# Kernel tuning notes

Hardware: AMD Instinct MI355X
Metric: run time of the kernel (lower is better)

The kernel has to match this reference:

```python
import jax, jax.numpy as jnp
import numpy as np
import math

N_LAYERS = 8
D = 1024
H = 16
DK = D // H
T = 1024
V = 32000
B = 2
DFF = 4 * D
EPS = 1e-5


def layernorm(x, scale, bias):
    mu = jnp.mean(x, axis=-1, keepdims=True)
    var = jnp.mean(jnp.square(x - mu), axis=-1, keepdims=True)
    return (x - mu) * jax.lax.rsqrt(var + EPS) * scale + bias


def setup_inputs() -> dict:
    key = jax.random.key(0)
    ks = jax.random.split(key, 32)
    s = 0.02
    rn = lambda k, shape: jax.random.normal(k, shape, dtype=jnp.float32) * s
    x = jax.random.randint(ks[0], (B, T), 0, V)
    return {
        "x": x,
        "inp_emb": rn(ks[1], (V, D)),
        "pos_emb": rn(ks[2], (T, D)),
        # per-layer weights stacked on leading layer axis; per-head wq/wk/wv are
        # concatenated along the output dim (mathematically identical to the
        # per-head nn.Linear list in the torch code)
        "wq": rn(ks[3], (N_LAYERS, D, D)), "bq": jnp.zeros((N_LAYERS, D), jnp.float32),
        "wk": rn(ks[4], (N_LAYERS, D, D)), "bk": jnp.zeros((N_LAYERS, D), jnp.float32),
        "wv": rn(ks[5], (N_LAYERS, D, D)), "bv": jnp.zeros((N_LAYERS, D), jnp.float32),
        "wo": rn(ks[6], (N_LAYERS, D, D)), "bo": jnp.zeros((N_LAYERS, D), jnp.float32),
        "w1": rn(ks[7], (N_LAYERS, D, DFF)), "b1": jnp.zeros((N_LAYERS, DFF), jnp.float32),
        "w2": rn(ks[8], (N_LAYERS, DFF, D)), "b2": jnp.zeros((N_LAYERS, D), jnp.float32),
        "ln1_s": jnp.ones((N_LAYERS, D), jnp.float32), "ln1_b": jnp.zeros((N_LAYERS, D), jnp.float32),
        "ln2_s": jnp.ones((N_LAYERS, D), jnp.float32), "ln2_b": jnp.zeros((N_LAYERS, D), jnp.float32),
        "lno_s": jnp.ones((D,), jnp.float32), "lno_b": jnp.zeros((D,), jnp.float32),
        "w_out": rn(ks[9], (D, V)),
    }


def reference(x, inp_emb, pos_emb, wq, bq, wk, bk, wv, bv, wo, bo,
              w1, b1, w2, b2, ln1_s, ln1_b, ln2_s, ln2_b, lno_s, lno_b, w_out):
    h = inp_emb[x] + pos_emb[jnp.arange(T)]            # [B,T,D]
    causal = jnp.tril(jnp.ones((T, T), dtype=bool))    # [T,T]
    scale = 1.0 / math.sqrt(DK)
    for i in range(N_LAYERS):
        # --- multi-head causal attention ---
        xn = layernorm(h, ln1_s[i], ln1_b[i])
        q = (xn @ wq[i] + bq[i]).reshape(B, T, H, DK)
        k = (xn @ wk[i] + bk[i]).reshape(B, T, H, DK)
        v = (xn @ wv[i] + bv[i]).reshape(B, T, H, DK)
        scores = jnp.einsum('bqhd,bkhd->bhqk', q, k) * scale
        scores = jnp.where(causal, scores, -jnp.inf)
        att = jax.nn.softmax(scores, axis=-1)           # [B,H,T,T]
        y = jnp.einsum('bhqk,bkhd->bqhd', att, v).reshape(B, T, D)
        h = h + y @ wo[i] + bo[i]
        # --- feed-forward ---
        xn = layernorm(h, ln2_s[i], ln2_b[i])
        h = h + jax.nn.gelu(xn @ w1[i] + b1[i], approximate=False) @ w2[i] + b2[i]
    h = layernorm(h, lno_s, lno_b)
    return h @ w_out                                    # logits [B,T,V]
```

## Files before the change

kernel.cpp:

```cpp
#include <hip/hip_runtime.h>
#include <cmath>

#define D_MODEL 1024
#define N_HEADS 16
#define DKH     64
#define SEQ_T   1024
#define BATCH   2
#define VOCAB   32000
#define DFF_    4096
#define NLAYERS 8

typedef __bf16 bf16x8 __attribute__((ext_vector_type(8)));
typedef __bf16 bf16x4v __attribute__((ext_vector_type(4)));
typedef float  f32x4  __attribute__((ext_vector_type(4)));

__device__ __forceinline__ float gelu_f(float x) {
    return 0.5f * x * (1.0f + erff(x * 0.70710678118654752f));
}

__device__ __forceinline__ void gload_lds16(const void* g, void* l) {
    __builtin_amdgcn_global_load_lds(
        (const __attribute__((address_space(1))) void*)g,
        (__attribute__((address_space(3))) void*)l, 16, 0, 0);
}

__global__ __launch_bounds__(256) void embed_kernel(
    const int* __restrict__ x, const float* __restrict__ inp_emb,
    const float* __restrict__ pos_emb, float* __restrict__ h)
{
    const int idx = blockIdx.x * 256 + threadIdx.x;
    const int bt  = idx >> 10;
    const int d   = idx & 1023;
    const int t   = bt & (SEQ_T - 1);
    const int tok = x[bt];
    h[idx] = inp_emb[(size_t)tok * D_MODEL + d] + pos_emb[(size_t)t * D_MODEL + d];
}

__global__ __launch_bounds__(256) void layernorm_kernel(
    const float* __restrict__ x, const float* __restrict__ sc,
    const float* __restrict__ bi, __bf16* __restrict__ o)
{
    const int row = blockIdx.x;
    const int tid = threadIdx.x;
    const int c   = tid * 4;
    const float4 v = *(const float4*)(x + (size_t)row * D_MODEL + c);
    float sum = v.x + v.y + v.z + v.w;
    float sq  = v.x * v.x + v.y * v.y + v.z * v.z + v.w * v.w;
    #pragma unroll
    for (int off = 32; off > 0; off >>= 1) {
        sum += __shfl_xor(sum, off);
        sq  += __shfl_xor(sq, off);
    }
    __shared__ float ssum[4], ssq[4];
    const int wave = tid >> 6, lane = tid & 63;
    if (lane == 0) { ssum[wave] = sum; ssq[wave] = sq; }
    __syncthreads();
    sum = ssum[0] + ssum[1] + ssum[2] + ssum[3];
    sq  = ssq[0]  + ssq[1]  + ssq[2]  + ssq[3];
    const float mu  = sum * (1.0f / D_MODEL);
    const float var = sq * (1.0f / D_MODEL) - mu * mu;
    const float rs  = rsqrtf(var + 1e-5f);
    const float4 s4 = *(const float4*)(sc + c);
    const float4 b4 = *(const float4*)(bi + c);
    bf16x4v ov;
    ov[0] = (__bf16)((v.x - mu) * rs * s4.x + b4.x);
    ov[1] = (__bf16)((v.y - mu) * rs * s4.y + b4.y);
    ov[2] = (__bf16)((v.z - mu) * rs * s4.z + b4.z);
    ov[3] = (__bf16)((v.w - mu) * rs * s4.w + b4.w);
    *(bf16x4v*)(o + (size_t)row * D_MODEL + c) = ov;
}

__global__ __launch_bounds__(256) void prep_layer_kernel(
    const float* __restrict__ wq, const float* __restrict__ wk,
    const float* __restrict__ wv, const float* __restrict__ wo,
    const float* __restrict__ w1, const float* __restrict__ w2,
    const float* __restrict__ bq, const float* __restrict__ bk,
    const float* __restrict__ bv,
    __bf16* __restrict__ wqkvT, __bf16* __restrict__ woT,
    __bf16* __restrict__ w1T, __bf16* __restrict__ w2T,
    float* __restrict__ bqkv)
{
    __shared__ __bf16 tile[32][36];
    const int b   = blockIdx.x;
    const int tid = threadIdx.x;

    if (b >= 12288) {
        const int j = (b - 12288) * 256 + tid;
        bqkv[j] = (j < 1024) ? bq[j] : (j < 2048 ? bk[j - 1024] : bv[j - 2048]);
        return;
    }

    const float* in;
    __bf16* out;
    int K, N, kb0, nb0;
    if (b < 4096) {
        const int w = b >> 10, t = b & 1023;
        K = 1024; N = 1024; kb0 = (t >> 5) * 32; nb0 = (t & 31) * 32;
        in  = (w == 0) ? wq : (w == 1) ? wk : (w == 2) ? wv : wo;
        out = (w == 3) ? woT : wqkvT + (size_t)w * 1024 * 1024;
    } else if (b < 8192) {
        const int t = b - 4096;
        K = 1024; N = 4096; kb0 = (t >> 7) * 32; nb0 = (t & 127) * 32;
        in = w1; out = w1T;
    } else {
        const int t = b - 8192;
        K = 4096; N = 1024; kb0 = (t >> 5) * 32; nb0 = (t & 31) * 32;
        in = w2; out = w2T;
    }

    {
        const int rr = tid >> 3, c4 = (tid & 7) * 4;
        const float4 v = *(const float4*)(in + (size_t)(kb0 + rr) * N + nb0 + c4);
        tile[rr][c4 + 0] = (__bf16)v.x;
        tile[rr][c4 + 1] = (__bf16)v.y;
        tile[rr][c4 + 2] = (__bf16)v.z;
        tile[rr][c4 + 3] = (__bf16)v.w;
    }
    __syncthreads();
    {
        const int cc = tid >> 3, r4 = (tid & 7) * 4;
        bf16x4v ov;
        ov[0] = tile[r4 + 0][cc];
        ov[1] = tile[r4 + 1][cc];
        ov[2] = tile[r4 + 2][cc];
        ov[3] = tile[r4 + 3][cc];
        *(bf16x4v*)(out + (size_t)(nb0 + cc) * K + kb0 + r4) = ov;
    }
}

__global__ __launch_bounds__(256) void wout_tr_kernel(
    const float* __restrict__ in, __bf16* __restrict__ out)
{
    __shared__ __bf16 tile[32][36];
    const int tid = threadIdx.x;
    const int nb0 = (blockIdx.x >> 5) * 32;
    const int kb0 = (blockIdx.x & 31) * 32;
    {
        const int rr = tid >> 3, c4 = (tid & 7) * 4;
        const float4 v = *(const float4*)(in + (size_t)(kb0 + rr) * VOCAB + nb0 + c4);
        tile[rr][c4 + 0] = (__bf16)v.x;
        tile[rr][c4 + 1] = (__bf16)v.y;
        tile[rr][c4 + 2] = (__bf16)v.z;
        tile[rr][c4 + 3] = (__bf16)v.w;
    }
    __syncthreads();
    {
        const int cc = tid >> 3, r4 = (tid & 7) * 4;
        bf16x4v ov;
        ov[0] = tile[r4 + 0][cc];
        ov[1] = tile[r4 + 1][cc];
        ov[2] = tile[r4 + 2][cc];
        ov[3] = tile[r4 + 3][cc];
        *(bf16x4v*)(out + (size_t)(nb0 + cc) * D_MODEL + kb0 + r4) = ov;
    }
}

template <int BN_T, int EPI, typename OutT, bool NT = false>
__global__ __launch_bounds__(256) void gemm_bt(
    const __bf16* __restrict__ A, const __bf16* __restrict__ Bt,
    const float* __restrict__ bias, const float* __restrict__ res,
    OutT* __restrict__ C, int M, int N, int K)
{
    constexpr int NF  = BN_T / 32;
    constexpr int NCB = BN_T / 8;
    __shared__ __bf16 As[128 * 64];
    __shared__ __bf16 Bs[BN_T * 64];

    const int tid  = threadIdx.x;
    const int wave = tid >> 6;
    const int lane = tid & 63;
    const int r    = lane & 15;
    const int kb   = lane >> 4;
    const int wm   = wave >> 1;
    const int wn   = wave & 1;

    const int ntm = gridDim.x;
    const int nwg = ntm * gridDim.y;
    int bid = blockIdx.y * ntm + blockIdx.x;
    if ((nwg & 7) == 0) bid = (bid & 7) * (nwg >> 3) + (bid >> 3);
    const int bm = (bid % ntm) * 128;
    const int bn = (bid / ntm) * BN_T;

    const int srow = lane >> 3;
    const int sg   = lane & 7;

    f32x4 acc[4][NF] = {};

    for (int k0 = 0; k0 < K; k0 += 64) {
        #pragma unroll
        for (int i = 0; i < 4; ++i) {
            const int c    = i * 4 + wave;
            const int row  = c * 8 + srow;
            const int scol = (sg ^ (row & 7)) * 8;
            gload_lds16(A + (size_t)(bm + row) * K + k0 + scol, &As[c * 512]);
        }
        #pragma unroll
        for (int i = 0; i < NCB / 4; ++i) {
            const int c    = i * 4 + wave;
            const int row  = c * 8 + srow;
            const int scol = (sg ^ (row & 7)) * 8;
            gload_lds16(Bt + (size_t)(bn + row) * K + k0 + scol, &Bs[c * 512]);
        }
        __syncthreads();

        #pragma unroll
        for (int s = 0; s < 2; ++s) {
            bf16x8 af[4];
            #pragma unroll
            for (int m = 0; m < 4; ++m) {
                const int row = wm * 64 + m * 16 + r;
                const int g   = (s * 4 + kb) ^ (row & 7);
                af[m] = *(const bf16x8*)&As[row * 64 + g * 8];
            }
            #pragma unroll
            for (int n = 0; n < NF; ++n) {
                const int row = wn * (NF * 16) + n * 16 + r;
                const int g   = (s * 4 + kb) ^ (row & 7);
                const bf16x8 bfr = *(const bf16x8*)&Bs[row * 64 + g * 8];
                #pragma unroll
                for (int m = 0; m < 4; ++m)
                    acc[m][n] = __builtin_amdgcn_mfma_f32_16x16x32_bf16(af[m], bfr, acc[m][n], 0, 0, 0);
            }
        }
        __syncthreads();
    }

    #pragma unroll
    for (int m = 0; m < 4; ++m) {
        const int row = bm + wm * 64 + m * 16 + kb * 4;
        #pragma unroll
        for (int n = 0; n < NF; ++n) {
            const int col = bn + wn * (NF * 16) + n * 16 + r;
            const float bv = bias ? bias[col] : 0.0f;
            #pragma unroll
            for (int rg = 0; rg < 4; ++rg) {
                float v = acc[m][n][rg] + bv;
                if constexpr (EPI == 1) v += res[(size_t)(row + rg) * N + col];
                if constexpr (EPI == 2) v = gelu_f(v);
                if constexpr (NT) {
                    __builtin_nontemporal_store((OutT)v, &C[(size_t)(row + rg) * N + col]);
                } else {
                    C[(size_t)(row + rg) * N + col] = (OutT)v;
                }
            }
        }
    }
}

struct AttnState {
    float m[4];
    float l[4];
    f32x4 yacc[4];
};

template <bool MASK>
__device__ __forceinline__ void attn_tile_step(
    AttnState& st, const bf16x8 (&qf)[2], int q0, int kt,
    int wave, int r, int kb,
    const __bf16 (*K_lds)[72], const __bf16 (*V_lds)[72],
    __bf16 (*P_row)[72])
{
    f32x4 sacc[4] = {};
    #pragma unroll
    for (int kc = 0; kc < 2; ++kc) {
        #pragma unroll
        for (int g = 0; g < 4; ++g) {
            const bf16x8 kf = *(const bf16x8*)&K_lds[g * 16 + r][kc * 32 + kb * 8];
            sacc[g] = __builtin_amdgcn_mfma_f32_16x16x32_bf16(qf[kc], kf, sacc[g], 0, 0, 0);
        }
    }

    float s[4][4], p[4][4];
    #pragma unroll
    for (int g = 0; g < 4; ++g) {
        #pragma unroll
        for (int rg = 0; rg < 4; ++rg) {
            if constexpr (MASK) {
                const int key = kt * 64 + g * 16 + r;
                const int qq  = q0 + wave * 16 + kb * 4 + rg;
                s[g][rg] = (key <= qq) ? sacc[g][rg] * 0.125f : -INFINITY;
            } else {
                s[g][rg] = sacc[g][rg] * 0.125f;
            }
        }
    }

    float mt[4];
    #pragma unroll
    for (int rg = 0; rg < 4; ++rg)
        mt[rg] = fmaxf(fmaxf(s[0][rg], s[1][rg]), fmaxf(s[2][rg], s[3][rg]));
    #pragma unroll
    for (int off = 1; off < 16; off <<= 1) {
        #pragma unroll
        for (int rg = 0; rg < 4; ++rg) mt[rg] = fmaxf(mt[rg], __shfl_xor(mt[rg], off));
    }

    bool grow = false;
    #pragma unroll
    for (int rg = 0; rg < 4; ++rg) grow |= (mt[rg] > st.m[rg] + 8.0f);
    if (__any(grow)) {
        #pragma unroll
        for (int rg = 0; rg < 4; ++rg) {
            const float mn   = fmaxf(st.m[rg], mt[rg]);
            const float corr = __expf(st.m[rg] - mn);
            st.l[rg] *= corr;
            st.m[rg]  = mn;
            #pragma unroll
            for (int n = 0; n < 4; ++n) st.yacc[n][rg] *= corr;
        }
    }

    float psum[4];
    #pragma unroll
    for (int rg = 0; rg < 4; ++rg) {
        psum[rg] = 0.0f;
        #pragma unroll
        for (int g = 0; g < 4; ++g) {
            p[g][rg] = __expf(s[g][rg] - st.m[rg]);
            psum[rg] += p[g][rg];
        }
    }
    #pragma unroll
    for (int off = 1; off < 16; off <<= 1) {
        #pragma unroll
        for (int rg = 0; rg < 4; ++rg) psum[rg] += __shfl_xor(psum[rg], off);
    }
    #pragma unroll
    for (int rg = 0; rg < 4; ++rg) st.l[rg] += psum[rg];

    #pragma unroll
    for (int g = 0; g < 4; ++g) {
        #pragma unroll
        for (int rg = 0; rg < 4; ++rg)
            P_row[kb * 4 + rg][g * 16 + r] = (__bf16)p[g][rg];
    }
    const bf16x8 pa0 = *(const bf16x8*)&P_row[r][kb * 8];
    const bf16x8 pa1 = *(const bf16x8*)&P_row[r][32 + kb * 8];

    #pragma unroll
    for (int n = 0; n < 4; ++n) {
        const int vrow = n * 16 + r;
        const int swz  = (vrow >> 3) & 7;
        const bf16x8 vf0 = *(const bf16x8*)&V_lds[vrow][(kb ^ swz) * 8];
        st.yacc[n] = __builtin_amdgcn_mfma_f32_16x16x32_bf16(pa0, vf0, st.yacc[n], 0, 0, 0);
    }
    #pragma unroll
    for (int n = 0; n < 4; ++n) {
        const int vrow = n * 16 + r;
        const int swz  = (vrow >> 3) & 7;
        const bf16x8 vf1 = *(const bf16x8*)&V_lds[vrow][((kb + 4) ^ swz) * 8];
        st.yacc[n] = __builtin_amdgcn_mfma_f32_16x16x32_bf16(pa1, vf1, st.yacc[n], 0, 0, 0);
    }
}

__global__ __launch_bounds__(256) void attn_mfma_kernel(
    const __bf16* __restrict__ qkv, __bf16* __restrict__ y)
{
    constexpr int QS = 3 * D_MODEL;
    __shared__ __align__(16) __bf16 K_lds[64][72];
    __shared__ __align__(16) __bf16 V_lds[64][72];
    __shared__ __align__(16) __bf16 P_lds[4][16][72];

    const int tid  = threadIdx.x;
    const int wave = tid >> 6;
    const int lane = tid & 63;
    const int r    = lane & 15;
    const int kb   = lane >> 4;

    const int ip  = blockIdx.x;
    const int q0A = ip * 64;
    const int q0B = (15 - ip) * 64;
    const int b   = blockIdx.y >> 4;
    const int h   = blockIdx.y & 15;

    const __bf16* qp = qkv + (size_t)b * SEQ_T * QS + h * DKH;
    const __bf16* kp = qp + D_MODEL;
    const __bf16* vp = qp + 2 * D_MODEL;
    __bf16* yp = y + (size_t)b * SEQ_T * D_MODEL + h * DKH;

    bf16x8 qfA[2], qfB[2];
    {
        const int qrA = q0A + wave * 16 + r;
        const int qrB = q0B + wave * 16 + r;
        #pragma unroll
        for (int kc = 0; kc < 2; ++kc) {
            qfA[kc] = *(const bf16x8*)(qp + (size_t)qrA * QS + kc * 32 + kb * 8);
            qfB[kc] = *(const bf16x8*)(qp + (size_t)qrB * QS + kc * 32 + kb * 8);
        }
    }

    AttnState stA, stB;
    #pragma unroll
    for (int rg = 0; rg < 4; ++rg) {
        stA.m[rg] = -INFINITY; stA.l[rg] = 0.0f;
        stB.m[rg] = -INFINITY; stB.l[rg] = 0.0f;
    }
    #pragma unroll
    for (int n = 0; n < 4; ++n) { stA.yacc[n] = {}; stB.yacc[n] = {}; }

    const int skey = tid >> 2;
    const int sg16 = (tid & 3) * 16;

    const int ntiles = 16 - ip;
    for (int kt = 0; kt < ntiles; ++kt) {
        {
            const size_t go = (size_t)(kt * 64 + skey) * QS;
            *(bf16x8*)&K_lds[skey][sg16]     = *(const bf16x8*)(kp + go + sg16);
            *(bf16x8*)&K_lds[skey][sg16 + 8] = *(const bf16x8*)(kp + go + sg16 + 8);
            const bf16x8 v0 = *(const bf16x8*)(vp + go + sg16);
            const bf16x8 v1 = *(const bf16x8*)(vp + go + sg16 + 8);
            const int swz0 = ((sg16 >> 3) & 7) * 8;
            const int swz1 = (((sg16 + 8) >> 3) & 7) * 8;
            #pragma unroll
            for (int j = 0; j < 8; ++j)
                V_lds[sg16 + j][skey ^ swz0] = v0[j];
            #pragma unroll
            for (int j = 0; j < 8; ++j)
                V_lds[sg16 + 8 + j][skey ^ swz1] = v1[j];
        }
        __syncthreads();

        if (kt == ntiles - 1)
            attn_tile_step<true >(stB, qfB, q0B, kt, wave, r, kb, K_lds, V_lds, P_lds[wave]);
        else
            attn_tile_step<false>(stB, qfB, q0B, kt, wave, r, kb, K_lds, V_lds, P_lds[wave]);
        if (kt <= ip) {
            if (kt == ip)
                attn_tile_step<true >(stA, qfA, q0A, kt, wave, r, kb, K_lds, V_lds, P_lds[wave]);
            else
                attn_tile_step<false>(stA, qfA, q0A, kt, wave, r, kb, K_lds, V_lds, P_lds[wave]);
        }
        __syncthreads();
    }

    float invA[4], invB[4];
    #pragma unroll
    for (int rg = 0; rg < 4; ++rg) {
        invA[rg] = 1.0f / stA.l[rg];
        invB[rg] = 1.0f / stB.l[rg];
    }
    #pragma unroll
    for (int n = 0; n < 4; ++n) {
        #pragma unroll
        for (int rg = 0; rg < 4; ++rg) {
            const int rowA = q0A + wave * 16 + kb * 4 + rg;
            const int rowB = q0B + wave * 16 + kb * 4 + rg;
            yp[(size_t)rowA * D_MODEL + n * 16 + r] = (__bf16)(stA.yacc[n][rg] * invA[rg]);
            yp[(size_t)rowB * D_MODEL + n * 16 + r] = (__bf16)(stB.yacc[n][rg] * invB[rg]);
        }
    }
}

extern "C" void kernel_launch(void* const* d_in, const int* in_sizes, int n_in,
                              void* d_out, int out_size, void* d_ws, size_t ws_size,
                              hipStream_t stream)
{
    const int*   x       = (const int*)  d_in[0];
    const float* inp_emb = (const float*)d_in[1];
    const float* pos_emb = (const float*)d_in[2];
    const float* wq = (const float*)d_in[3];
    const float* bq = (const float*)d_in[4];
    const float* wk = (const float*)d_in[5];
    const float* bk = (const float*)d_in[6];
    const float* wv = (const float*)d_in[7];
    const float* bv = (const float*)d_in[8];
    const float* wo = (const float*)d_in[9];
    const float* bo = (const float*)d_in[10];
    const float* w1 = (const float*)d_in[11];
    const float* b1 = (const float*)d_in[12];
    const float* w2 = (const float*)d_in[13];
    const float* b2 = (const float*)d_in[14];
    const float* ln1_s = (const float*)d_in[15];
    const float* ln1_b = (const float*)d_in[16];
    const float* ln2_s = (const float*)d_in[17];
    const float* ln2_b = (const float*)d_in[18];
    const float* lno_s = (const float*)d_in[19];
    const float* lno_b = (const float*)d_in[20];
    const float* w_out = (const float*)d_in[21];

    const int M = BATCH * SEQ_T;
    const size_t MB = 1u << 20;

    char* w = (char*)d_ws;
    float*  h     = (float*) (w + 0);
    __bf16* xn    = (__bf16*)(w + 8  * MB);
    __bf16* yb    = (__bf16*)(w + 12 * MB);
    __bf16* sh    = (__bf16*)(w + 16 * MB);
    __bf16* wqkvT = (__bf16*)(w + 32 * MB);
    __bf16* woT   = (__bf16*)(w + 38 * MB);
    __bf16* w1T   = (__bf16*)(w + 40 * MB);
    __bf16* w2T   = (__bf16*)(w + 48 * MB);
    float*  bqkv  = (float*) (w + 56 * MB);
    __bf16* woutT = (__bf16*)(w + 57 * MB);

    embed_kernel<<<dim3(M * D_MODEL / 256), 256, 0, stream>>>(x, inp_emb, pos_emb, h);

    for (int i = 0; i < NLAYERS; ++i) {
        const size_t wOff  = (size_t)i * D_MODEL * D_MODEL;
        const size_t w1Off = (size_t)i * D_MODEL * DFF_;

        prep_layer_kernel<<<dim3(12300), 256, 0, stream>>>(
            wq + wOff, wk + wOff, wv + wOff, wo + wOff, w1 + w1Off, w2 + w1Off,
            bq + i * D_MODEL, bk + i * D_MODEL, bv + i * D_MODEL,
            wqkvT, woT, w1T, w2T, bqkv);

        layernorm_kernel<<<dim3(M), 256, 0, stream>>>(h, ln1_s + i * D_MODEL, ln1_b + i * D_MODEL, xn);
        gemm_bt<64, 0, __bf16><<<dim3(M / 128, 3 * D_MODEL / 64), 256, 0, stream>>>(
            xn, wqkvT, bqkv, nullptr, sh, M, 3 * D_MODEL, D_MODEL);
        attn_mfma_kernel<<<dim3(8, BATCH * N_HEADS), 256, 0, stream>>>(sh, yb);
        gemm_bt<64, 1, float><<<dim3(M / 128, D_MODEL / 64), 256, 0, stream>>>(
            yb, woT, bo + i * D_MODEL, h, h, M, D_MODEL, D_MODEL);
        layernorm_kernel<<<dim3(M), 256, 0, stream>>>(h, ln2_s + i * D_MODEL, ln2_b + i * D_MODEL, xn);
        gemm_bt<128, 2, __bf16><<<dim3(M / 128, DFF_ / 128), 256, 0, stream>>>(
            xn, w1T, b1 + i * DFF_, nullptr, sh, M, DFF_, D_MODEL);
        gemm_bt<64, 1, float><<<dim3(M / 128, D_MODEL / 64), 256, 0, stream>>>(
            sh, w2T, b2 + i * D_MODEL, h, h, M, D_MODEL, DFF_);
    }

    wout_tr_kernel<<<dim3((VOCAB / 32) * 32), 256, 0, stream>>>(w_out, woutT);
    layernorm_kernel<<<dim3(M), 256, 0, stream>>>(h, lno_s, lno_b, xn);
    gemm_bt<128, 0, float, true><<<dim3(M / 128, VOCAB / 128), 256, 0, stream>>>(
        xn, woutT, nullptr, nullptr, (float*)d_out, M, VOCAB, D_MODEL);
}
```

Before: 1.675 ms.

## Fuse layernorm into weight prep, stage logits via LDS, prefetch attention K/V

Merges the per-layer weight transpose/convert kernel with the first layernorm, and folds the w_out transpose into the layer-0 prep launch, removing separate launches. The output-logits GEMM epilogue now stages results through shared memory so each row is written with coalesced 16-byte nontemporal stores instead of scattered scalar stores. The attention kernel register-prefetches the next K/V tile while the current one is being computed. The trade-off is larger launches and higher register pressure in attention.

```diff
diff --git a/kernel.cpp b/kernel.cpp
--- a/kernel.cpp
+++ b/kernel.cpp
@@ -36,13 +36,11 @@
     h[idx] = inp_emb[(size_t)tok * D_MODEL + d] + pos_emb[(size_t)t * D_MODEL + d];
 }
 
-__global__ __launch_bounds__(256) void layernorm_kernel(
+__device__ __forceinline__ void ln_row(
     const float* __restrict__ x, const float* __restrict__ sc,
-    const float* __restrict__ bi, __bf16* __restrict__ o)
-{
-    const int row = blockIdx.x;
-    const int tid = threadIdx.x;
-    const int c   = tid * 4;
+    const float* __restrict__ bi, __bf16* __restrict__ o, int row, int tid)
+{
+    const int c = tid * 4;
     const float4 v = *(const float4*)(x + (size_t)row * D_MODEL + c);
     float sum = v.x + v.y + v.z + v.w;
     float sq  = v.x * v.x + v.y * v.y + v.z * v.z + v.w * v.w;
@@ -70,7 +68,16 @@
     *(bf16x4v*)(o + (size_t)row * D_MODEL + c) = ov;
 }
 
-__global__ __launch_bounds__(256) void prep_layer_kernel(
+__global__ __launch_bounds__(256) void layernorm_kernel(
+    const float* __restrict__ x, const float* __restrict__ sc,
+    const float* __restrict__ bi, __bf16* __restrict__ o)
+{
+    ln_row(x, sc, bi, o, blockIdx.x, threadIdx.x);
+}
+
+__global__ __launch_bounds__(256) void prep_ln_kernel(
+    const float* __restrict__ h, const float* __restrict__ ln_s,
+    const float* __restrict__ ln_b, __bf16* __restrict__ xn,
     const float* __restrict__ wq, const float* __restrict__ wk,
     const float* __restrict__ wv, const float* __restrict__ wo,
     const float* __restrict__ w1, const float* __restrict__ w2,
@@ -78,34 +85,44 @@
     const float* __restrict__ bv,
     __bf16* __restrict__ wqkvT, __bf16* __restrict__ woT,
     __bf16* __restrict__ w1T, __bf16* __restrict__ w2T,
-    float* __restrict__ bqkv)
-{
-    __shared__ __bf16 tile[32][36];
+    float* __restrict__ bqkv,
+    const float* __restrict__ wout, __bf16* __restrict__ woutT)
+{
+    const int tid = threadIdx.x;
     const int b   = blockIdx.x;
-    const int tid = threadIdx.x;
-
-    if (b >= 12288) {
-        const int j = (b - 12288) * 256 + tid;
+
+    if (b < 2048) {
+        ln_row(h, ln_s, ln_b, xn, b, tid);
+        return;
+    }
+    const int pb = b - 2048;
+    if (pb >= 12288 && pb < 12300) {
+        const int j = (pb - 12288) * 256 + tid;
         bqkv[j] = (j < 1024) ? bq[j] : (j < 2048 ? bk[j - 1024] : bv[j - 2048]);
         return;
     }
 
+    __shared__ __bf16 tile[32][36];
     const float* in;
     __bf16* out;
     int K, N, kb0, nb0;
-    if (b < 4096) {
-        const int w = b >> 10, t = b & 1023;
+    if (pb < 4096) {
+        const int w = pb >> 10, t = pb & 1023;
         K = 1024; N = 1024; kb0 = (t >> 5) * 32; nb0 = (t & 31) * 32;
         in  = (w == 0) ? wq : (w == 1) ? wk : (w == 2) ? wv : wo;
         out = (w == 3) ? woT : wqkvT + (size_t)w * 1024 * 1024;
-    } else if (b < 8192) {
-        const int t = b - 4096;
+    } else if (pb < 8192) {
+        const int t = pb - 4096;
         K = 1024; N = 4096; kb0 = (t >> 7) * 32; nb0 = (t & 127) * 32;
         in = w1; out = w1T;
-    } else {
-        const int t = b - 8192;
+    } else if (pb < 12288) {
+        const int t = pb - 8192;
         K = 4096; N = 1024; kb0 = (t >> 5) * 32; nb0 = (t & 31) * 32;
         in = w2; out = w2T;
+    } else {
+        const int t = pb - 12300;
+        K = 1024; N = VOCAB; kb0 = (t & 31) * 32; nb0 = (t >> 5) * 32;
+        in = wout; out = woutT;
     }
 
     {
@@ -128,33 +145,6 @@
     }
 }
 
-__global__ __launch_bounds__(256) void wout_tr_kernel(
-    const float* __restrict__ in, __bf16* __restrict__ out)
-{
-    __shared__ __bf16 tile[32][36];
-    const int tid = threadIdx.x;
-    const int nb0 = (blockIdx.x >> 5) * 32;
-    const int kb0 = (blockIdx.x & 31) * 32;
-    {
-        const int rr = tid >> 3, c4 = (tid & 7) * 4;
-        const float4 v = *(const float4*)(in + (size_t)(kb0 + rr) * VOCAB + nb0 + c4);
-        tile[rr][c4 + 0] = (__bf16)v.x;
-        tile[rr][c4 + 1] = (__bf16)v.y;
-        tile[rr][c4 + 2] = (__bf16)v.z;
-        tile[rr][c4 + 3] = (__bf16)v.w;
-    }
-    __syncthreads();
-    {
-        const int cc = tid >> 3, r4 = (tid & 7) * 4;
-        bf16x4v ov;
-        ov[0] = tile[r4 + 0][cc];
-        ov[1] = tile[r4 + 1][cc];
-        ov[2] = tile[r4 + 2][cc];
-        ov[3] = tile[r4 + 3][cc];
-        *(bf16x4v*)(out + (size_t)(nb0 + cc) * D_MODEL + kb0 + r4) = ov;
-    }
-}
-
 template <int BN_T, int EPI, typename OutT, bool NT = false>
 __global__ __launch_bounds__(256) void gemm_bt(
     const __bf16* __restrict__ A, const __bf16* __restrict__ Bt,
@@ -163,8 +153,9 @@
 {
     constexpr int NF  = BN_T / 32;
     constexpr int NCB = BN_T / 8;
-    __shared__ __bf16 As[128 * 64];
-    __shared__ __bf16 Bs[BN_T * 64];
+    __shared__ __align__(16) char smem[(128 + BN_T) * 64 * 2];
+    __bf16* As = (__bf16*)smem;
+    __bf16* Bs = As + 128 * 64;
 
     const int tid  = threadIdx.x;
     const int wave = tid >> 6;
@@ -225,6 +216,37 @@
         __syncthreads();
     }
 
+    if constexpr (NT) {
+        float* Cs = (float*)smem;
+        #pragma unroll
+        for (int cchunk = 0; cchunk < 4; ++cchunk) {
+            if (wm == (cchunk >> 1)) {
+                #pragma unroll
+                for (int mm = 0; mm < 2; ++mm) {
+                    const int m = (cchunk & 1) * 2 + mm;
+                    #pragma unroll
+                    for (int n = 0; n < NF; ++n) {
+                        const int col = wn * (NF * 16) + n * 16 + r;
+                        const float bv = bias ? bias[bn + col] : 0.0f;
+                        #pragma unroll
+                        for (int rg = 0; rg < 4; ++rg)
+                            Cs[(mm * 16 + kb * 4 + rg) * 132 + col] = acc[m][n][rg] + bv;
+                    }
+                }
+            }
+            __syncthreads();
+            const int rrow = tid >> 3, g8 = tid & 7;
+            const size_t grow = (size_t)(bm + cchunk * 32 + rrow) * N + bn;
+            #pragma unroll
+            for (int j = 0; j < 4; ++j) {
+                const f32x4 v = *(const f32x4*)&Cs[rrow * 132 + j * 32 + g8 * 4];
+                __builtin_nontemporal_store(v, (f32x4*)((float*)C + grow + j * 32 + g8 * 4));
+            }
+            __syncthreads();
+        }
+        return;
+    }
+
     #pragma unroll
     for (int m = 0; m < 4; ++m) {
         const int row = bm + wm * 64 + m * 16 + kb * 4;
@@ -237,11 +259,7 @@
                 float v = acc[m][n][rg] + bv;
                 if constexpr (EPI == 1) v += res[(size_t)(row + rg) * N + col];
                 if constexpr (EPI == 2) v = gelu_f(v);
-                if constexpr (NT) {
-                    __builtin_nontemporal_store((OutT)v, &C[(size_t)(row + rg) * N + col]);
-                } else {
-                    C[(size_t)(row + rg) * N + col] = (OutT)v;
-                }
+                C[(size_t)(row + rg) * N + col] = (OutT)v;
             }
         }
     }
@@ -400,25 +418,38 @@
 
     const int skey = tid >> 2;
     const int sg16 = (tid & 3) * 16;
+    const int swz0 = ((sg16 >> 3) & 7) * 8;
+    const int swz1 = (((sg16 + 8) >> 3) & 7) * 8;
 
     const int ntiles = 16 - ip;
+
+    bf16x8 kr0, kr1, vr0, vr1;
+    {
+        const size_t go = (size_t)skey * QS;
+        kr0 = *(const bf16x8*)(kp + go + sg16);
+        kr1 = *(const bf16x8*)(kp + go + sg16 + 8);
+        vr0 = *(const bf16x8*)(vp + go + sg16);
+        vr1 = *(const bf16x8*)(vp + go + sg16 + 8);
+    }
+
     for (int kt = 0; kt < ntiles; ++kt) {
-        {
-            const size_t go = (size_t)(kt * 64 + skey) * QS;
-            *(bf16x8*)&K_lds[skey][sg16]     = *(const bf16x8*)(kp + go + sg16);
-            *(bf16x8*)&K_lds[skey][sg16 + 8] = *(const bf16x8*)(kp + go + sg16 + 8);
-            const bf16x8 v0 = *(const bf16x8*)(vp + go + sg16);
-            const bf16x8 v1 = *(const bf16x8*)(vp + go + sg16 + 8);
-            const int swz0 = ((sg16 >> 3) & 7) * 8;
-            const int swz1 = (((sg16 + 8) >> 3) & 7) * 8;
-            #pragma unroll
-            for (int j = 0; j < 8; ++j)
-                V_lds[sg16 + j][skey ^ swz0] = v0[j];
-            #pragma unroll
-            for (int j = 0; j < 8; ++j)
-                V_lds[sg16 + 8 + j][skey ^ swz1] = v1[j];
-        }
+        *(bf16x8*)&K_lds[skey][sg16]     = kr0;
+        *(bf16x8*)&K_lds[skey][sg16 + 8] = kr1;
+        #pragma unroll
+        for (int j = 0; j < 8; ++j)
+            V_lds[sg16 + j][skey ^ swz0] = vr0[j];
+        #pragma unroll
+        for (int j = 0; j < 8; ++j)
+            V_lds[sg16 + 8 + j][skey ^ swz1] = vr1[j];
         __syncthreads();
+
+        if (kt + 1 < ntiles) {
+            const size_t go = (size_t)((kt + 1) * 64 + skey) * QS;
+            kr0 = *(const bf16x8*)(kp + go + sg16);
+            kr1 = *(const bf16x8*)(kp + go + sg16 + 8);
+            vr0 = *(const bf16x8*)(vp + go + sg16);
+            vr1 = *(const bf16x8*)(vp + go + sg16 + 8);
+        }
 
         if (kt == ntiles - 1)
             attn_tile_step<true >(stB, qfB, q0B, kt, wave, r, kb, K_lds, V_lds, P_lds[wave]);
@@ -499,12 +530,14 @@
         const size_t wOff  = (size_t)i * D_MODEL * D_MODEL;
         const size_t w1Off = (size_t)i * D_MODEL * DFF_;
 
-        prep_layer_kernel<<<dim3(12300), 256, 0, stream>>>(
+        const int nblk = 2048 + 12300 + (i == 0 ? 32000 : 0);
+        prep_ln_kernel<<<dim3(nblk), 256, 0, stream>>>(
+            h, ln1_s + i * D_MODEL, ln1_b + i * D_MODEL, xn,
             wq + wOff, wk + wOff, wv + wOff, wo + wOff, w1 + w1Off, w2 + w1Off,
             bq + i * D_MODEL, bk + i * D_MODEL, bv + i * D_MODEL,
-            wqkvT, woT, w1T, w2T, bqkv);
-
-        layernorm_kernel<<<dim3(M), 256, 0, stream>>>(h, ln1_s + i * D_MODEL, ln1_b + i * D_MODEL, xn);
+            wqkvT, woT, w1T, w2T, bqkv,
+            (i == 0) ? w_out : nullptr, woutT);
+
         gemm_bt<64, 0, __bf16><<<dim3(M / 128, 3 * D_MODEL / 64), 256, 0, stream>>>(
             xn, wqkvT, bqkv, nullptr, sh, M, 3 * D_MODEL, D_MODEL);
         attn_mfma_kernel<<<dim3(8, BATCH * N_HEADS), 256, 0, stream>>>(sh, yb);
@@ -517,7 +550,6 @@
             sh, w2T, b2 + i * D_MODEL, h, h, M, D_MODEL, DFF_);
     }
 
-    wout_tr_kernel<<<dim3((VOCAB / 32) * 32), 256, 0, stream>>>(w_out, woutT);
     layernorm_kernel<<<dim3(M), 256, 0, stream>>>(h, lno_s, lno_b, xn);
     gemm_bt<128, 0, float, true><<<dim3(M / 128, VOCAB / 128), 256, 0, stream>>>(
         xn, woutT, nullptr, nullptr, (float*)d_out, M, VOCAB, D_MODEL);
```

New measurement: 1.661 ms. No clear change (-0.9%).
